# Kernel optimization log

Measured on AMD Instinct MI355X. Metric: run time of the kernel, lower is better.

The kernel has to match this reference:

```python
import jax, jax.numpy as jnp
import numpy as np
from jax import lax

# Model hyperparameters (from module source: D_state=2, Expand=1; mamba-ssm defaults)
B_, C_, H_, W_ = 16, 128, 96, 96
D_MODEL = C_
D_INNER = 1 * D_MODEL          # expand = 1
D_STATE = 2
DT_RANK = (D_MODEL + 15) // 16  # ceil(d_model/16) = 8
D_CONV = 4
OUT_C = 128
LN_EPS = 1e-5


def setup_inputs() -> dict:
    key = jax.random.key(0)
    ks = jax.random.split(key, 10)
    s = 0.02
    x = jax.random.normal(ks[0], (B_, C_, H_, W_), dtype=jnp.float32)
    in_proj_w = jax.random.normal(ks[1], (2 * D_INNER, D_MODEL), dtype=jnp.float32) * s
    conv_w = jax.random.normal(ks[2], (D_INNER, 1, D_CONV), dtype=jnp.float32) * s
    conv_b = jnp.zeros((D_INNER,), dtype=jnp.float32)
    x_proj_w = jax.random.normal(ks[3], (DT_RANK + 2 * D_STATE, D_INNER), dtype=jnp.float32) * s
    dt_proj_w = jax.random.normal(ks[4], (D_INNER, DT_RANK), dtype=jnp.float32) * s
    # softplus^{-1}(0.01) so initial dt ~ 0.01 (standard mamba init)
    dt_proj_b = jnp.full((D_INNER,), float(np.log(np.expm1(0.01))), dtype=jnp.float32)
    A_log = jnp.log(jnp.broadcast_to(jnp.arange(1, D_STATE + 1, dtype=jnp.float32), (D_INNER, D_STATE)))
    D_param = jnp.ones((D_INNER,), dtype=jnp.float32)
    out_proj_w = jax.random.normal(ks[5], (OUT_C, D_INNER), dtype=jnp.float32) * s
    ln_gamma = jnp.ones((OUT_C,), dtype=jnp.float32)
    ln_beta = jnp.zeros((OUT_C,), dtype=jnp.float32)
    return {
        "x": x, "in_proj_w": in_proj_w, "conv_w": conv_w, "conv_b": conv_b,
        "x_proj_w": x_proj_w, "dt_proj_w": dt_proj_w, "dt_proj_b": dt_proj_b,
        "A_log": A_log, "D_param": D_param, "out_proj_w": out_proj_w,
        "ln_gamma": ln_gamma, "ln_beta": ln_beta,
    }


def _ssm_cha(x, in_proj_w, conv_w, conv_b, x_proj_w, dt_proj_w, dt_proj_b,
             A_log, D_param, out_proj_w, ln_gamma, ln_beta):
    b, c, h, w = x.shape
    L = h * w
    tokens = x.transpose(0, 2, 3, 1).reshape(b, L, c)  # [b, L, d_model]

    # in_proj -> (x_in, z)
    xz = jnp.einsum("bld,ed->ble", tokens, in_proj_w)  # [b, L, 2*d_inner]
    x_in, z = jnp.split(xz, 2, axis=-1)

    # causal depthwise conv1d over L, then SiLU
    xc = x_in.transpose(0, 2, 1)  # [b, d_inner, L]
    xc = lax.conv_general_dilated(
        xc, conv_w, window_strides=(1,), padding=[(D_CONV - 1, 0)],
        dimension_numbers=("NCH", "OIH", "NCH"), feature_group_count=D_INNER,
    ) + conv_b[None, :, None]
    x_in = jax.nn.silu(xc).transpose(0, 2, 1)  # [b, L, d_inner]

    # x_proj -> (dt, B, C)
    x_dbl = jnp.einsum("bld,ed->ble", x_in, x_proj_w)
    dt = x_dbl[..., :DT_RANK]
    Bc = x_dbl[..., DT_RANK:DT_RANK + D_STATE]         # [b, L, n]
    Cc = x_dbl[..., DT_RANK + D_STATE:]                # [b, L, n]
    dt = jax.nn.softplus(jnp.einsum("blr,dr->bld", dt, dt_proj_w) + dt_proj_b)

    # selective scan (diagonal A) via associative scan over L
    A = -jnp.exp(A_log)                                # [d_inner, n]
    dA = jnp.exp(dt[..., None] * A)                    # [b, L, d_inner, n]
    dBx = dt[..., None] * Bc[:, :, None, :] * x_in[..., None]

    def combine(e1, e2):
        a1, b1 = e1
        a2, b2 = e2
        return a1 * a2, a2 * b1 + b2

    _, hstate = lax.associative_scan(combine, (dA, dBx), axis=1)  # [b, L, d, n]
    y = jnp.sum(hstate * Cc[:, :, None, :], axis=-1) + D_param * x_in  # [b, L, d]

    y = y * jax.nn.silu(z)
    out = jnp.einsum("bld,od->blo", y, out_proj_w)     # [b, L, out_c]

    # LayerNorm over out_c
    mu = jnp.mean(out, axis=-1, keepdims=True)
    var = jnp.mean(jnp.square(out - mu), axis=-1, keepdims=True)
    out = (out - mu) * lax.rsqrt(var + LN_EPS) * ln_gamma + ln_beta

    return out.reshape(b, h, w, OUT_C).transpose(0, 3, 1, 2)


def reference(x, in_proj_w, conv_w, conv_b, x_proj_w, dt_proj_w, dt_proj_b,
              A_log, D_param, out_proj_w, ln_gamma, ln_beta):
    return _ssm_cha(x, in_proj_w, conv_w, conv_b, x_proj_w, dt_proj_w, dt_proj_b,
                    A_log, D_param, out_proj_w, ln_gamma, ln_beta)
```

## Files before the change

kernel.cpp:

```cpp
#include <hip/hip_runtime.h>
#include <hip/hip_bf16.h>

#define B_N 16
#define L_N 9216
#define LT64 144

typedef __attribute__((ext_vector_type(8))) short short8;
typedef __attribute__((ext_vector_type(4))) float floatx4;

__device__ __forceinline__ float bfu(unsigned short u) {
  return __uint_as_float(((unsigned int)u) << 16);
}
__device__ __forceinline__ unsigned short fbf(float f) {
  __hip_bfloat16 h = __float2bfloat16(f);
  return *(unsigned short*)&h;
}

__global__ __launch_bounds__(256) void k_prep(const float* __restrict__ w1,
                                              const float* __restrict__ w2,
                                              __hip_bfloat16* __restrict__ w1bt,
                                              __hip_bfloat16* __restrict__ w2bt) {
  int i = blockIdx.x * 256 + threadIdx.x;
  if (i < 256 * 128) w1bt[i] = __float2bfloat16(w1[i]);
  if (i < 128 * 128) w2bt[i] = __float2bfloat16(w2[i]);
}

__global__ __launch_bounds__(512, 4) void k_inproj_conv(
    const float* __restrict__ x, const __hip_bfloat16* __restrict__ w1bt,
    const float* __restrict__ cw, const float* __restrict__ cb,
    const float* __restrict__ xpw,
    __hip_bfloat16* __restrict__ xinb, __hip_bfloat16* __restrict__ zb,
    float* __restrict__ xdblT) {
  __shared__ __align__(16) char smem1[16384];
  __shared__ __align__(16) char smem2[34816];
  unsigned short* xs = (unsigned short*)smem1;
  unsigned short* xe = (unsigned short*)smem2;
  float (*cvs)[68] = (float(*)[68])smem2;
  float (*red)[12][64] = (float(*)[12][64])smem2;

  int blk = blockIdx.x, b = blk / LT64, lt = blk % LT64, l0 = lt * 64;
  int t = threadIdx.x;
  int lane = t & 63, wv = t >> 6;
  int col = lane & 15, quad = lane >> 4;

  const float* xb = x + (size_t)b * 128 * L_N + l0 - 16;
#pragma unroll
  for (int i = 0; i < 5; ++i) {
    int idx = t + i * 512;
    int c = idx & 127, q = idx >> 7;
    float4 v = {0.f, 0.f, 0.f, 0.f};
    if (!(lt == 0 && q < 4)) v = *(const float4*)(xb + (size_t)c * L_N + q * 4);
    int ch = c >> 3, ce = c & 7;
    if (q < 4) {
#pragma unroll
      for (int j = 0; j < 4; ++j) {
        int l = q * 4 + j;
        xe[l * 128 + (((ch ^ (l & 7)) << 3) | ce)] = fbf(((const float*)&v)[j]);
      }
    } else {
#pragma unroll
      for (int j = 0; j < 4; ++j) {
        int l = q * 4 - 16 + j;
        xs[l * 128 + (((ch ^ (l & 7)) << 3) | ce)] = fbf(((const float*)&v)[j]);
      }
    }
  }

  int e0 = wv * 32;
  const __hip_bfloat16* wbp = w1bt + (size_t)(e0 + col) * 128 + quad * 8;
  floatx4 vzero = {0.f, 0.f, 0.f, 0.f};
  floatx4 acc[2][5];
#pragma unroll
  for (int mi = 0; mi < 2; ++mi)
#pragma unroll
    for (int ni = 0; ni < 5; ++ni) acc[mi][ni] = vzero;
  short8 a0 = *(const short8*)(wbp);
  short8 a1 = *(const short8*)(wbp + 16 * 128);
  __syncthreads();

#pragma unroll
  for (int ks = 0; ks < 4; ++ks) {
    short8 n0, n1;
    if (ks < 3) {
      n0 = *(const short8*)(wbp + (ks + 1) * 32);
      n1 = *(const short8*)(wbp + 16 * 128 + (ks + 1) * 32);
    }
    short8 bfr[5];
    bfr[0] = *(const short8*)&xe[col * 128 + (((ks * 4 + quad) ^ (col & 7)) << 3)];
#pragma unroll
    for (int ni = 1; ni < 5; ++ni) {
      int row = (ni - 1) * 16 + col;
      bfr[ni] = *(const short8*)&xs[row * 128 + (((ks * 4 + quad) ^ (row & 7)) << 3)];
    }
#pragma unroll
    for (int ni = 0; ni < 5; ++ni) {
      acc[0][ni] = __builtin_amdgcn_mfma_f32_16x16x32_bf16(a0, bfr[ni], acc[0][ni], 0, 0, 0);
      acc[1][ni] = __builtin_amdgcn_mfma_f32_16x16x32_bf16(a1, bfr[ni], acc[1][ni], 0, 0, 0);
    }
    a0 = n0; a1 = n1;
  }
  __syncthreads();

  if (wv >= 4) {
    __hip_bfloat16* zbase = zb + ((size_t)b * 128 + (e0 - 128)) * L_N + l0;
#pragma unroll
    for (int mi = 0; mi < 2; ++mi)
#pragma unroll
      for (int r = 0; r < 4; ++r) {
        int dr = mi * 16 + quad * 4 + r;
#pragma unroll
        for (int ni = 1; ni < 5; ++ni)
          zbase[(size_t)dr * L_N + (ni - 1) * 16 + col] = __float2bfloat16(acc[mi][ni][r]);
      }
  } else {
#pragma unroll
    for (int mi = 0; mi < 2; ++mi)
#pragma unroll
      for (int r = 0; r < 4; ++r) {
        int d = e0 + mi * 16 + quad * 4 + r;
        if (col >= 13) cvs[d][col - 13] = acc[mi][0][r];
#pragma unroll
        for (int ni = 1; ni < 5; ++ni) cvs[d][3 + (ni - 1) * 16 + col] = acc[mi][ni][r];
      }
  }
  __syncthreads();

  float part[12];
#pragma unroll
  for (int m = 0; m < 12; ++m) part[m] = 0.f;
  for (int dd = 0; dd < 16; ++dd) {
    int d = wv * 16 + dd;
    float v = cb[d] + cw[d * 4 + 0] * cvs[d][lane] + cw[d * 4 + 1] * cvs[d][lane + 1]
                    + cw[d * 4 + 2] * cvs[d][lane + 2] + cw[d * 4 + 3] * cvs[d][lane + 3];
    v = v / (1.f + __expf(-v));
    xinb[((size_t)b * 128 + d) * L_N + l0 + lane] = __float2bfloat16(v);
#pragma unroll
    for (int m = 0; m < 12; ++m) part[m] += xpw[m * 128 + d] * v;
  }
  __syncthreads();
#pragma unroll
  for (int m = 0; m < 12; ++m) red[wv][m][lane] = part[m];
  __syncthreads();
  for (int idx = t; idx < 12 * 64; idx += 512) {
    int m = idx >> 6, l = idx & 63;
    float s = 0.f;
#pragma unroll
    for (int w8 = 0; w8 < 8; ++w8) s += red[w8][m][l];
    xdblT[((size_t)b * 12 + m) * L_N + l0 + l] = s;
  }
}

__global__ __launch_bounds__(256) void k_scan(
    const float* __restrict__ xdblT, const float* __restrict__ dtw,
    const float* __restrict__ dtb, const float* __restrict__ alog,
    const float* __restrict__ dpar,
    const __hip_bfloat16* __restrict__ xinb, const __hip_bfloat16* __restrict__ zb,
    __hip_bfloat16* __restrict__ yb) {
  __shared__ float agg[4][4];
  __shared__ float carry[2];
  int blk = blockIdx.x, b = blk >> 7, d = blk & 127;
  int t = threadIdx.x, lane = t & 63, wv = t >> 6;
  float A0 = -__expf(alog[2 * d]), A1 = -__expf(alog[2 * d + 1]);
  float Dv = dpar[d], dtbv = dtb[d];
  float w[8];
#pragma unroll
  for (int i = 0; i < 8; ++i) w[i] = dtw[d * 8 + i];
  if (t == 0) { carry[0] = 0.f; carry[1] = 0.f; }
  __syncthreads();
  const float* xdT = xdblT + (size_t)b * 12 * L_N;
  const unsigned short* xi = (const unsigned short*)xinb + ((size_t)b * 128 + d) * L_N;
  const unsigned short* zr = (const unsigned short*)zb + ((size_t)b * 128 + d) * L_N;
  unsigned short* yo = (unsigned short*)yb + ((size_t)b * 128 + d) * L_N;
  for (int it = 0; it < 9; ++it) {
    int lb = it * 1024 + t * 4;
    float4 q[12];
#pragma unroll
    for (int m = 0; m < 12; ++m) q[m] = *(const float4*)(xdT + (size_t)m * L_N + lb);
    ushort4 xu = *(const ushort4*)(xi + lb);
    ushort4 zu = *(const ushort4*)(zr + lb);
    float xv[4] = {bfu(xu.x), bfu(xu.y), bfu(xu.z), bfu(xu.w)};
    float zv[4] = {bfu(zu.x), bfu(zu.y), bfu(zu.z), bfu(zu.w)};
    float A0p[4], X0p[4], A1p[4], X1p[4];
#pragma unroll
    for (int j = 0; j < 4; ++j) {
      float dtp = dtbv;
#pragma unroll
      for (int m = 0; m < 8; ++m) dtp += w[m] * ((const float*)&q[m])[j];
      float dt = (dtp > 15.f) ? dtp : __logf(1.f + __expf(dtp));
      float a0 = __expf(dt * A0), a1 = __expf(dt * A1);
      float dtx = dt * xv[j];
      float x0 = dtx * ((const float*)&q[8])[j];
      float x1 = dtx * ((const float*)&q[9])[j];
      if (j == 0) { A0p[0] = a0; X0p[0] = x0; A1p[0] = a1; X1p[0] = x1; }
      else {
        A0p[j] = a0 * A0p[j - 1]; X0p[j] = a0 * X0p[j - 1] + x0;
        A1p[j] = a1 * A1p[j - 1]; X1p[j] = a1 * X1p[j - 1] + x1;
      }
    }
    float wA0 = A0p[3], wX0 = X0p[3], wA1 = A1p[3], wX1 = X1p[3];
#pragma unroll
    for (int off = 1; off < 64; off <<= 1) {
      float pA0 = __shfl_up(wA0, off, 64), pX0 = __shfl_up(wX0, off, 64);
      float pA1 = __shfl_up(wA1, off, 64), pX1 = __shfl_up(wX1, off, 64);
      if (lane >= off) {
        wX0 += wA0 * pX0; wA0 *= pA0;
        wX1 += wA1 * pX1; wA1 *= pA1;
      }
    }
    if (lane == 63) { agg[wv][0] = wA0; agg[wv][1] = wX0; agg[wv][2] = wA1; agg[wv][3] = wX1; }
    float eA0 = __shfl_up(wA0, 1, 64), eX0 = __shfl_up(wX0, 1, 64);
    float eA1 = __shfl_up(wA1, 1, 64), eX1 = __shfl_up(wX1, 1, 64);
    if (lane == 0) { eA0 = 1.f; eX0 = 0.f; eA1 = 1.f; eX1 = 0.f; }
    __syncthreads();
    float h0 = carry[0], h1 = carry[1];
    for (int jw = 0; jw < wv; ++jw) {
      h0 = agg[jw][0] * h0 + agg[jw][1];
      h1 = agg[jw][2] * h1 + agg[jw][3];
    }
    h0 = eA0 * h0 + eX0;
    h1 = eA1 * h1 + eX1;
    __syncthreads();
    if (t == 255) { carry[0] = A0p[3] * h0 + X0p[3]; carry[1] = A1p[3] * h1 + X1p[3]; }
    ushort4 yu;
    unsigned short* yp = (unsigned short*)&yu;
#pragma unroll
    for (int j = 0; j < 4; ++j) {
      float hh0 = A0p[j] * h0 + X0p[j];
      float hh1 = A1p[j] * h1 + X1p[j];
      float y = hh0 * ((const float*)&q[10])[j] + hh1 * ((const float*)&q[11])[j] + Dv * xv[j];
      y *= zv[j] / (1.f + __expf(-zv[j]));
      yp[j] = fbf(y);
    }
    *(ushort4*)(yo + lb) = yu;
  }
}

__global__ __launch_bounds__(256) void k_outln(
    const __hip_bfloat16* __restrict__ yb, const __hip_bfloat16* __restrict__ w2bt,
    const float* __restrict__ gam, const float* __restrict__ bet,
    float* __restrict__ out) {
  __shared__ unsigned short st[128][68];
  __shared__ __hip_bfloat16 yts[64 * 128];
  __shared__ float red_s[4][64], red_q[4][64];
  __shared__ float gs[128], bs[128];
  int blk = blockIdx.x, b = blk / LT64, lt = blk % LT64, l0 = lt * 64;
  int t = threadIdx.x;
  if (t < 128) { gs[t] = gam[t]; bs[t] = bet[t]; }
  const unsigned short* ybb = (const unsigned short*)yb + (size_t)b * 128 * L_N + l0;
#pragma unroll
  for (int i = 0; i < 8; ++i) {
    int idx = t + i * 256;
    int dd = idx >> 4, l4 = (idx & 15) * 4;
    ushort4 v = *(const ushort4*)(ybb + (size_t)dd * L_N + l4);
    *(ushort4*)&st[dd][l4] = v;
  }
  __syncthreads();
#pragma unroll
  for (int p = 0; p < 4; ++p) {
    int gi = t + p * 256;
    int l = gi & 63, ch = gi >> 6;
    short8 c;
#pragma unroll
    for (int j = 0; j < 8; ++j) c[j] = (short)st[ch * 8 + j][l];
    *(short8*)&yts[l * 128 + ((ch ^ (l & 7)) * 8)] = c;
  }
  int lane = t & 63, wv = t >> 6;
  int col = lane & 15, quad = lane >> 4;
  int o0 = wv * 32;
  short8 afr[2][4];
#pragma unroll
  for (int mi = 0; mi < 2; ++mi)
#pragma unroll
    for (int ks = 0; ks < 4; ++ks)
      afr[mi][ks] = *(const short8*)(w2bt + (size_t)(o0 + mi * 16 + col) * 128 + ks * 32 + quad * 8);
  floatx4 vzero = {0.f, 0.f, 0.f, 0.f};
  floatx4 acc[2][4];
#pragma unroll
  for (int mi = 0; mi < 2; ++mi)
#pragma unroll
    for (int ni = 0; ni < 4; ++ni) acc[mi][ni] = vzero;
  __syncthreads();
#pragma unroll
  for (int ks = 0; ks < 4; ++ks) {
    short8 bfr[4];
#pragma unroll
    for (int ni = 0; ni < 4; ++ni) {
      int row = ni * 16 + col;
      bfr[ni] = *(const short8*)&yts[row * 128 + (((ks * 4 + quad) ^ (row & 7)) * 8)];
    }
#pragma unroll
    for (int mi = 0; mi < 2; ++mi)
#pragma unroll
      for (int ni = 0; ni < 4; ++ni)
        acc[mi][ni] = __builtin_amdgcn_mfma_f32_16x16x32_bf16(afr[mi][ks], bfr[ni], acc[mi][ni], 0, 0, 0);
  }
  float s[4], q[4];
#pragma unroll
  for (int ni = 0; ni < 4; ++ni) {
    float ss = 0.f, qq = 0.f;
#pragma unroll
    for (int mi = 0; mi < 2; ++mi)
#pragma unroll
      for (int r = 0; r < 4; ++r) {
        float v = acc[mi][ni][r];
        ss += v; qq += v * v;
      }
    ss += __shfl_xor(ss, 16, 64); ss += __shfl_xor(ss, 32, 64);
    qq += __shfl_xor(qq, 16, 64); qq += __shfl_xor(qq, 32, 64);
    s[ni] = ss; q[ni] = qq;
  }
  if (quad == 0) {
#pragma unroll
    for (int ni = 0; ni < 4; ++ni) {
      red_s[wv][ni * 16 + col] = s[ni];
      red_q[wv][ni * 16 + col] = q[ni];
    }
  }
  __syncthreads();
  float mu[4], rstd[4];
#pragma unroll
  for (int ni = 0; ni < 4; ++ni) {
    int li = ni * 16 + col;
    float ts = red_s[0][li] + red_s[1][li] + red_s[2][li] + red_s[3][li];
    float tq = red_q[0][li] + red_q[1][li] + red_q[2][li] + red_q[3][li];
    float m = ts * (1.f / 128.f);
    float var = tq * (1.f / 128.f) - m * m;
    mu[ni] = m;
    rstd[ni] = rsqrtf(var + 1e-5f);
  }
  float* ob = out + (size_t)b * 128 * L_N;
#pragma unroll
  for (int mi = 0; mi < 2; ++mi)
#pragma unroll
    for (int r = 0; r < 4; ++r) {
      int o = o0 + mi * 16 + quad * 4 + r;
      float g = gs[o], bb = bs[o];
#pragma unroll
      for (int ni = 0; ni < 4; ++ni)
        ob[(size_t)o * L_N + l0 + ni * 16 + col] = (acc[mi][ni][r] - mu[ni]) * rstd[ni] * g + bb;
    }
}

extern "C" void kernel_launch(void* const* d_in, const int* in_sizes, int n_in,
                              void* d_out, int out_size, void* d_ws, size_t ws_size,
                              hipStream_t stream) {
  const float* x    = (const float*)d_in[0];
  const float* w1   = (const float*)d_in[1];
  const float* cw   = (const float*)d_in[2];
  const float* cb   = (const float*)d_in[3];
  const float* xpw  = (const float*)d_in[4];
  const float* dtw  = (const float*)d_in[5];
  const float* dtb  = (const float*)d_in[6];
  const float* alog = (const float*)d_in[7];
  const float* dpar = (const float*)d_in[8];
  const float* w2   = (const float*)d_in[9];
  const float* gam  = (const float*)d_in[10];
  const float* bet  = (const float*)d_in[11];
  float* out = (float*)d_out;

  float* ws = (float*)d_ws;
  const size_t NBL = (size_t)B_N * 128 * L_N;
  float* xdblT = ws;
  __hip_bfloat16* xinb = (__hip_bfloat16*)(ws + (size_t)B_N * 12 * L_N);
  __hip_bfloat16* zb   = xinb + NBL;
  __hip_bfloat16* yb   = zb + NBL;
  __hip_bfloat16* w1bt = yb + NBL;
  __hip_bfloat16* w2bt = w1bt + 256 * 128;

  k_prep<<<128, 256, 0, stream>>>(w1, w2, w1bt, w2bt);
  k_inproj_conv<<<B_N * LT64, 512, 0, stream>>>(x, w1bt, cw, cb, xpw, xinb, zb, xdblT);
  k_scan<<<B_N * 128, 256, 0, stream>>>(xdblT, dtw, dtb, alog, dpar, xinb, zb, yb);
  k_outln<<<B_N * LT64, 256, 0, stream>>>(yb, w2bt, gam, bet, out);
}
```

Measured before the change: 296.1 us.

## Precompute dt projection and softplus in inproj kernel, pass fp16 dt to scan

The dt_proj matvec and softplus move from the scan kernel into the in_proj/conv kernel, which already holds the x_proj results in shared memory. dt is written as a per-channel fp16 tensor. The scan kernel now reads only the four B/C rows plus that dt stream, instead of twelve x_proj rows. This cuts shared-row loads and per-element arithmetic in the scan, at the cost of writing and reading an extra full-size fp16 [B,128,L] buffer through global memory and a small precision loss on dt.

```diff
diff --git a/kernel.cpp b/kernel.cpp
--- a/kernel.cpp
+++ b/kernel.cpp
@@ -1,5 +1,6 @@
 #include <hip/hip_runtime.h>
 #include <hip/hip_bf16.h>
+#include <hip/hip_fp16.h>
 
 #define B_N 16
 #define L_N 9216
@@ -14,6 +15,14 @@
 __device__ __forceinline__ unsigned short fbf(float f) {
   __hip_bfloat16 h = __float2bfloat16(f);
   return *(unsigned short*)&h;
+}
+__device__ __forceinline__ unsigned short fh(float f) {
+  __half h = __float2half(f);
+  return *(unsigned short*)&h;
+}
+__device__ __forceinline__ float hfu(unsigned short u) {
+  __half h = *(__half*)&u;
+  return __half2float(h);
 }
 
 __global__ __launch_bounds__(256) void k_prep(const float* __restrict__ w1,
@@ -28,9 +37,10 @@
 __global__ __launch_bounds__(512, 4) void k_inproj_conv(
     const float* __restrict__ x, const __hip_bfloat16* __restrict__ w1bt,
     const float* __restrict__ cw, const float* __restrict__ cb,
-    const float* __restrict__ xpw,
+    const float* __restrict__ xpw, const float* __restrict__ dtw,
+    const float* __restrict__ dtb,
     __hip_bfloat16* __restrict__ xinb, __hip_bfloat16* __restrict__ zb,
-    float* __restrict__ xdblT) {
+    float* __restrict__ xdbl4, unsigned short* __restrict__ dth) {
   __shared__ __align__(16) char smem1[16384];
   __shared__ __align__(16) char smem2[34816];
   unsigned short* xs = (unsigned short*)smem1;
@@ -146,14 +156,23 @@
     float s = 0.f;
 #pragma unroll
     for (int w8 = 0; w8 < 8; ++w8) s += red[w8][m][l];
-    xdblT[((size_t)b * 12 + m) * L_N + l0 + l] = s;
+    red[0][m][l] = s;
+    if (m >= 8) xdbl4[((size_t)b * 4 + (m - 8)) * L_N + l0 + l] = s;
+  }
+  __syncthreads();
+  for (int dd = 0; dd < 16; ++dd) {
+    int d = wv * 16 + dd;
+    float p = dtb[d];
+#pragma unroll
+    for (int r = 0; r < 8; ++r) p += dtw[d * 8 + r] * red[0][r][lane];
+    float dt = (p > 15.f) ? p : __logf(1.f + __expf(p));
+    dth[((size_t)b * 128 + d) * L_N + l0 + lane] = fh(dt);
   }
 }
 
 __global__ __launch_bounds__(256) void k_scan(
-    const float* __restrict__ xdblT, const float* __restrict__ dtw,
-    const float* __restrict__ dtb, const float* __restrict__ alog,
-    const float* __restrict__ dpar,
+    const float* __restrict__ xdbl4, const unsigned short* __restrict__ dth,
+    const float* __restrict__ alog, const float* __restrict__ dpar,
     const __hip_bfloat16* __restrict__ xinb, const __hip_bfloat16* __restrict__ zb,
     __hip_bfloat16* __restrict__ yb) {
   __shared__ float agg[4][4];
@@ -161,36 +180,33 @@
   int blk = blockIdx.x, b = blk >> 7, d = blk & 127;
   int t = threadIdx.x, lane = t & 63, wv = t >> 6;
   float A0 = -__expf(alog[2 * d]), A1 = -__expf(alog[2 * d + 1]);
-  float Dv = dpar[d], dtbv = dtb[d];
-  float w[8];
-#pragma unroll
-  for (int i = 0; i < 8; ++i) w[i] = dtw[d * 8 + i];
+  float Dv = dpar[d];
   if (t == 0) { carry[0] = 0.f; carry[1] = 0.f; }
   __syncthreads();
-  const float* xdT = xdblT + (size_t)b * 12 * L_N;
+  const float* xdT = xdbl4 + (size_t)b * 4 * L_N;
+  const unsigned short* dtp_ = dth + ((size_t)b * 128 + d) * L_N;
   const unsigned short* xi = (const unsigned short*)xinb + ((size_t)b * 128 + d) * L_N;
   const unsigned short* zr = (const unsigned short*)zb + ((size_t)b * 128 + d) * L_N;
   unsigned short* yo = (unsigned short*)yb + ((size_t)b * 128 + d) * L_N;
   for (int it = 0; it < 9; ++it) {
     int lb = it * 1024 + t * 4;
-    float4 q[12];
-#pragma unroll
-    for (int m = 0; m < 12; ++m) q[m] = *(const float4*)(xdT + (size_t)m * L_N + lb);
+    float4 q[4];
+#pragma unroll
+    for (int m = 0; m < 4; ++m) q[m] = *(const float4*)(xdT + (size_t)m * L_N + lb);
+    ushort4 du = *(const ushort4*)(dtp_ + lb);
     ushort4 xu = *(const ushort4*)(xi + lb);
     ushort4 zu = *(const ushort4*)(zr + lb);
+    float dtv[4] = {hfu(du.x), hfu(du.y), hfu(du.z), hfu(du.w)};
     float xv[4] = {bfu(xu.x), bfu(xu.y), bfu(xu.z), bfu(xu.w)};
     float zv[4] = {bfu(zu.x), bfu(zu.y), bfu(zu.z), bfu(zu.w)};
     float A0p[4], X0p[4], A1p[4], X1p[4];
 #pragma unroll
     for (int j = 0; j < 4; ++j) {
-      float dtp = dtbv;
-#pragma unroll
-      for (int m = 0; m < 8; ++m) dtp += w[m] * ((const float*)&q[m])[j];
-      float dt = (dtp > 15.f) ? dtp : __logf(1.f + __expf(dtp));
+      float dt = dtv[j];
       float a0 = __expf(dt * A0), a1 = __expf(dt * A1);
       float dtx = dt * xv[j];
-      float x0 = dtx * ((const float*)&q[8])[j];
-      float x1 = dtx * ((const float*)&q[9])[j];
+      float x0 = dtx * ((const float*)&q[0])[j];
+      float x1 = dtx * ((const float*)&q[1])[j];
       if (j == 0) { A0p[0] = a0; X0p[0] = x0; A1p[0] = a1; X1p[0] = x1; }
       else {
         A0p[j] = a0 * A0p[j - 1]; X0p[j] = a0 * X0p[j - 1] + x0;
@@ -227,7 +243,7 @@
     for (int j = 0; j < 4; ++j) {
       float hh0 = A0p[j] * h0 + X0p[j];
       float hh1 = A1p[j] * h1 + X1p[j];
-      float y = hh0 * ((const float*)&q[10])[j] + hh1 * ((const float*)&q[11])[j] + Dv * xv[j];
+      float y = hh0 * ((const float*)&q[2])[j] + hh1 * ((const float*)&q[3])[j] + Dv * xv[j];
       y *= zv[j] / (1.f + __expf(-zv[j]));
       yp[j] = fbf(y);
     }
@@ -360,15 +376,17 @@
 
   float* ws = (float*)d_ws;
   const size_t NBL = (size_t)B_N * 128 * L_N;
-  float* xdblT = ws;
-  __hip_bfloat16* xinb = (__hip_bfloat16*)(ws + (size_t)B_N * 12 * L_N);
+  float* xdbl4 = ws;
+  unsigned short* dth = (unsigned short*)(ws + (size_t)B_N * 4 * L_N);
+  __hip_bfloat16* xinb = (__hip_bfloat16*)(dth + NBL);
   __hip_bfloat16* zb   = xinb + NBL;
   __hip_bfloat16* yb   = zb + NBL;
   __hip_bfloat16* w1bt = yb + NBL;
   __hip_bfloat16* w2bt = w1bt + 256 * 128;
 
   k_prep<<<128, 256, 0, stream>>>(w1, w2, w1bt, w2bt);
-  k_inproj_conv<<<B_N * LT64, 512, 0, stream>>>(x, w1bt, cw, cb, xpw, xinb, zb, xdblT);
-  k_scan<<<B_N * 128, 256, 0, stream>>>(xdblT, dtw, dtb, alog, dpar, xinb, zb, yb);
+  k_inproj_conv<<<B_N * LT64, 512, 0, stream>>>(x, w1bt, cw, cb, xpw, dtw, dtb,
+                                                xinb, zb, xdbl4, dth);
+  k_scan<<<B_N * 128, 256, 0, stream>>>(xdbl4, dth, alog, dpar, xinb, zb, yb);
   k_outln<<<B_N * LT64, 256, 0, stream>>>(yb, w2bt, gam, bet, out);
 }
```

Result: no change. 300.7 us (+1.5%).
